# Performance work log

Measured on AMD Instinct MI355X. Metric: run time of the kernel, lower is better.

Reference implementation:

```python
import jax, jax.numpy as jnp
import numpy as np

B = 64
H_FS = W_FS = 56
IN_DIM, OUT_DIM, NUM_HEADS = 96, 192, 2
HEAD_DIM = OUT_DIM // NUM_HEADS  # 96
STRIDE_Q, STRIDE_KV = (2, 2), (4, 4)
REL_RANGE = 2 * (H_FS // STRIDE_Q[0]) - 1  # 55
LN_EPS = 1e-5


def setup_inputs() -> dict:
    key = jax.random.key(0)
    ks = jax.random.split(key, 12)
    N = H_FS * W_FS + 1  # +1 cls token
    s = 0.02
    d = {
        "hidden_states": jax.random.normal(ks[0], (B, N, IN_DIM), jnp.float32),
        "Wq": jax.random.normal(ks[1], (IN_DIM, OUT_DIM), jnp.float32) * s,
        "bq": jnp.zeros((OUT_DIM,), jnp.float32),
        "Wk": jax.random.normal(ks[2], (IN_DIM, OUT_DIM), jnp.float32) * s,
        "bk": jnp.zeros((OUT_DIM,), jnp.float32),
        "Wv": jax.random.normal(ks[3], (IN_DIM, OUT_DIM), jnp.float32) * s,
        "bv": jnp.zeros((OUT_DIM,), jnp.float32),
        # depthwise pool convs: (C_out=C, C_in/groups=1, kh, kw)
        "pool_q_w": jax.random.normal(ks[4], (IN_DIM, 1, 3, 3), jnp.float32) * 0.1,
        "pool_k_w": jax.random.normal(ks[5], (IN_DIM, 1, 3, 3), jnp.float32) * 0.1,
        "pool_v_w": jax.random.normal(ks[6], (IN_DIM, 1, 3, 3), jnp.float32) * 0.1,
        "gq": jnp.ones((IN_DIM,), jnp.float32), "betaq": jnp.zeros((IN_DIM,), jnp.float32),
        "gk": jnp.ones((IN_DIM,), jnp.float32), "betak": jnp.zeros((IN_DIM,), jnp.float32),
        "gv": jnp.ones((IN_DIM,), jnp.float32), "betav": jnp.zeros((IN_DIM,), jnp.float32),
        "rel_h": jax.random.normal(ks[7], (REL_RANGE, HEAD_DIM), jnp.float32) * s,
        "rel_w": jax.random.normal(ks[8], (REL_RANGE, HEAD_DIM), jnp.float32) * s,
        "height": H_FS,
        "width": W_FS,
    }
    return d


def _layernorm(x, g, b):
    m = x.mean(-1, keepdims=True)
    v = ((x - m) ** 2).mean(-1, keepdims=True)
    return (x - m) * jax.lax.rsqrt(v + LN_EPS) * g + b


def _pool(x, w, stride, g, b, height, width):
    # x: (B, folds=1, N, C) with cls token first
    bsz, _, _, C = x.shape
    cls_tok, rest = x[:, :, :1], x[:, :, 1:]
    sp = rest.reshape(bsz, height, width, C).transpose(0, 3, 1, 2)  # (B, C, H, W)
    y = jax.lax.conv_general_dilated(
        sp, w, stride, [(1, 1), (1, 1)], feature_group_count=C,
        dimension_numbers=("NCHW", "OIHW", "NCHW"))
    hp, wp = y.shape[2], y.shape[3]
    y = y.reshape(bsz, 1, C, hp * wp).transpose(0, 1, 3, 2)  # (B, 1, N', C)
    y = jnp.concatenate([cls_tok, y], axis=2)
    return _layernorm(y, g, b), (hp, wp)


def _rel_idx(qn, kn):
    q_ratio = max(kn / qn, 1.0)
    k_ratio = max(qn / kn, 1.0)
    dist = (np.arange(qn)[:, None] * q_ratio - np.arange(kn)[None, :] * k_ratio
            + (kn - 1) * k_ratio)
    return dist.astype(np.int64)


def reference(hidden_states, Wq, bq, Wk, bk, Wv, bv, pool_q_w, pool_k_w, pool_v_w,
              gq, betaq, gk, betak, gv, betav, rel_h, rel_w, height, width):
    bsz, N, C = hidden_states.shape
    h = hidden_states.reshape(bsz, N, 1, C).transpose(0, 2, 1, 3)  # (B, folds=1, N, C)

    q, (qh, qw) = _pool(h, pool_q_w, STRIDE_Q, gq, betaq, height, width)
    k, (kh, kw) = _pool(h, pool_k_w, STRIDE_KV, gk, betak, height, width)
    v, _ = _pool(h, pool_v_w, STRIDE_KV, gv, betav, height, width)

    def proj(x, W, bias, n):
        x = x.transpose(0, 2, 1, 3).reshape(bsz, n, -1)
        x = x @ W + bias
        return x.reshape(bsz, n, NUM_HEADS, HEAD_DIM).transpose(0, 2, 1, 3)

    nq, nk = qh * qw + 1, kh * kw + 1
    q = proj(q, Wq, bq, nq)  # (B, H, nq, d)
    k = proj(k, Wk, bk, nk)
    v = proj(v, Wv, bv, nk)

    scale = HEAD_DIM ** -0.5
    attn = jnp.einsum("bhqd,bhkd->bhqk", q * scale, k)

    # decomposed spatial relative positional bias (cls offset = 1)
    Rh = rel_h[_rel_idx(qh, kh)]  # (qh, kh, d)
    Rw = rel_w[_rel_idx(qw, kw)]  # (qw, kw, d)
    rq = q[:, :, 1:].reshape(bsz, NUM_HEADS, qh, qw, HEAD_DIM)
    eh = jnp.einsum("byhwc,hkc->byhwk", rq, Rh)
    ew = jnp.einsum("byhwc,wkc->byhwk", rq, Rw)
    blk = (attn[:, :, 1:, 1:].reshape(bsz, NUM_HEADS, qh, qw, kh, kw)
           + eh[..., :, None] + ew[..., None, :])
    attn = attn.at[:, :, 1:, 1:].set(blk.reshape(bsz, NUM_HEADS, qh * qw, kh * kw))

    attn = jax.nn.softmax(attn, axis=-1)
    out = jnp.einsum("bhqk,bhkd->bhqd", attn, v)
    out = out.at[:, :, 1:].add(q[:, :, 1:])  # residual pooling (skip cls)
    return out.transpose(0, 2, 1, 3).reshape(bsz, nq, OUT_DIM)
```

## Files before the change

### kernel.cpp

```cpp
#include <hip/hip_runtime.h>
#include <hip/hip_bf16.h>
#include <hip/hip_fp16.h>

#define B_    64
#define HFS   56
#define CIN   96
#define NQ    785
#define NK    197
#define QW    28
#define KW    14
#define NTOT  3137
#define NQP   800
#define NKP   208
#define NKPV  224
#define VROWS 112
#define KSCL  0.10206207261596575f
#define LOG2E 1.4426950408889634f
#define KSCL2 (KSCL*LOG2E)

typedef __attribute__((ext_vector_type(8))) short short8;
typedef __attribute__((ext_vector_type(4))) short shortx4;
typedef __attribute__((ext_vector_type(4))) float floatx4;

__device__ __forceinline__ short f2s(float x) {
    __hip_bfloat16 h = __float2bfloat16(x);
    return *reinterpret_cast<short*>(&h);
}
__device__ __forceinline__ float s2f(short s) {
    __hip_bfloat16 h; *reinterpret_cast<short*>(&h) = s;
    return __bfloat162float(h);
}
__device__ __forceinline__ short8 ld8(const short* p) {
    return *reinterpret_cast<const short8*>(p);
}
__device__ __forceinline__ unsigned pkbf(float a, float b) {
    return (unsigned)(unsigned short)f2s(a) | ((unsigned)(unsigned short)f2s(b) << 16);
}
__device__ __forceinline__ unsigned pkhf(float a, float b) {
    __half2 h = __floats2half2_rn(a, b);
    return *reinterpret_cast<unsigned*>(&h);
}
__device__ __forceinline__ float hflo(unsigned w) {
    __half2 h = *reinterpret_cast<__half2*>(&w);
    return __half2float(__low2half(h));
}
__device__ __forceinline__ float hfhi(unsigned w) {
    __half2 h = *reinterpret_cast<__half2*>(&w);
    return __half2float(__high2half(h));
}

#define MFMA16(a,b,c) __builtin_amdgcn_mfma_f32_16x16x32_bf16((a),(b),(c),0,0,0)

__global__ void prep_kernel(const float* __restrict__ Wq, const float* __restrict__ Wk,
                            const float* __restrict__ Wv, const float* __restrict__ relh,
                            const float* __restrict__ relw,
                            const float* __restrict__ pqw, const float* __restrict__ pkw,
                            const float* __restrict__ pvw,
                            short* __restrict__ WTq, short* __restrict__ WTk,
                            short* __restrict__ WTv, short* __restrict__ relc,
                            short* __restrict__ vt,
                            float* __restrict__ cwqT, float* __restrict__ cwkT,
                            float* __restrict__ cwvT)
{
    int i = blockIdx.x * 256 + threadIdx.x;
    if (i < 18432)      { int o = i/96, c = i%96;              WTq[o*96+c] = f2s(Wq[c*192+o]); }
    else if (i < 36864) { int j = i-18432; int o=j/96,c=j%96;  WTk[o*96+c] = f2s(Wk[c*192+o]*KSCL2); }
    else if (i < 55296) { int j = i-36864; int o=j/96,c=j%96;  WTv[o*96+c] = f2s(Wv[c*192+o]); }
    else if (i < 66048) {
        int j = i - 55296;  int r = j/96, c = j%96;
        float v = (r < 54) ? relh[r*96+c] : ((r < 108) ? relw[(r-54)*96+c] : 0.f);
        relc[r*96+c] = f2s(v*LOG2E);
    } else if (i < 721408) {
        int j2 = i - 66048;
        int bh = j2 / 5120, r = j2 % 5120;
        int row, tok; short val;
        if (r < 3584) { row = 96 + r/224; tok = r%224;
                        val = (row == 96 && tok < NK) ? (short)0x3F80 : (short)0; }
        else          { int rr = r-3584; row = rr/16; tok = 208 + (rr%16); val = 0; }
        vt[((long)bh*VROWS + row)*NKPV + tok] = val;
    } else if (i < 724000) {
        int j = i - 721408;
        int w = j / 864, r = j % 864;
        int c = r / 9, off = r % 9;
        const float* src = (w == 0) ? pqw : (w == 1) ? pkw : pvw;
        float*       dst = (w == 0) ? cwqT : (w == 1) ? cwkT : cwvT;
        dst[off*96 + c] = src[c*9 + off];
    }
}

__device__ __forceinline__ void red16_2(float& s, float& ss) {
    #pragma unroll
    for (int off = 8; off >= 1; off >>= 1) {
        s  += __shfl_xor(s,  off, 16);
        ss += __shfl_xor(ss, off, 16);
    }
}

__device__ __forceinline__ void ln6_store(const float* x, float m, float r,
    const float* __restrict__ g, const float* __restrict__ beta,
    int c0, short* __restrict__ outp)
{
    float2 g0 = *reinterpret_cast<const float2*>(g + c0);
    float2 g1 = *reinterpret_cast<const float2*>(g + c0 + 2);
    float2 g2 = *reinterpret_cast<const float2*>(g + c0 + 4);
    float2 b0 = *reinterpret_cast<const float2*>(beta + c0);
    float2 b1 = *reinterpret_cast<const float2*>(beta + c0 + 2);
    float2 b2 = *reinterpret_cast<const float2*>(beta + c0 + 4);
    unsigned o0 = pkbf((x[0]-m)*r*g0.x + b0.x, (x[1]-m)*r*g0.y + b0.y);
    unsigned o1 = pkbf((x[2]-m)*r*g1.x + b1.x, (x[3]-m)*r*g1.y + b1.y);
    unsigned o2 = pkbf((x[4]-m)*r*g2.x + b2.x, (x[5]-m)*r*g2.y + b2.y);
    *reinterpret_cast<unsigned*>(outp)     = o0;
    *reinterpret_cast<unsigned*>(outp + 2) = o1;
    *reinterpret_cast<unsigned*>(outp + 4) = o2;
}

__device__ __forceinline__ void zero6(short* __restrict__ outp) {
    *reinterpret_cast<unsigned*>(outp)     = 0u;
    *reinterpret_cast<unsigned*>(outp + 2) = 0u;
    *reinterpret_cast<unsigned*>(outp + 4) = 0u;
}

__global__ __launch_bounds__(256) void pool_ln_kernel(
    const float* __restrict__ hs,
    const float* __restrict__ cwqT, const float* __restrict__ cwkT, const float* __restrict__ cwvT,
    const float* __restrict__ gq, const float* __restrict__ betaq,
    const float* __restrict__ gk, const float* __restrict__ betak,
    const float* __restrict__ gv, const float* __restrict__ betav,
    short* __restrict__ pq, short* __restrict__ pk, short* __restrict__ pv)
{
    const int wid  = threadIdx.x >> 6;
    const int lane = threadIdx.x & 63;
    const int sub  = lane >> 4;
    const int li   = lane & 15;
    const int c0   = li * 6;
    const int gid  = blockIdx.x * 4 + wid;
    const int b    = gid / 252;
    const int slot = gid % 252;
    const long hb  = (long)b * NTOT * CIN;

    if (slot < 200) {
        int t = slot*4 + sub;
        short* outp = pq + ((long)b*NQP + t)*CIN + c0;
        if (t >= NQ) { zero6(outp); return; }
        float x[6];
        #pragma unroll
        for (int i = 0; i < 6; ++i) x[i] = 0.f;
        if (t == 0) {
            const float* hp = hs + hb + c0;
            float2 a0 = *reinterpret_cast<const float2*>(hp);
            float2 a1 = *reinterpret_cast<const float2*>(hp + 2);
            float2 a2 = *reinterpret_cast<const float2*>(hp + 4);
            x[0]=a0.x; x[1]=a0.y; x[2]=a1.x; x[3]=a1.y; x[4]=a2.x; x[5]=a2.y;
        } else {
            int j = t - 1, oy = j / QW, ox = j % QW;
            #pragma unroll
            for (int dy = 0; dy < 3; ++dy) {
                int iy = oy*2 - 1 + dy;
                #pragma unroll
                for (int dx = 0; dx < 3; ++dx) {
                    int ix = ox*2 - 1 + dx;
                    if (iy >= 0 && iy < HFS && ix >= 0 && ix < HFS) {
                        const float* hp = hs + hb + (long)(1 + iy*HFS + ix)*CIN + c0;
                        const float* wp = cwqT + (dy*3+dx)*96 + c0;
                        float2 h0 = *reinterpret_cast<const float2*>(hp);
                        float2 h1 = *reinterpret_cast<const float2*>(hp + 2);
                        float2 h2 = *reinterpret_cast<const float2*>(hp + 4);
                        float2 w0 = *reinterpret_cast<const float2*>(wp);
                        float2 w1 = *reinterpret_cast<const float2*>(wp + 2);
                        float2 w2 = *reinterpret_cast<const float2*>(wp + 4);
                        x[0] = fmaf(h0.x, w0.x, x[0]); x[1] = fmaf(h0.y, w0.y, x[1]);
                        x[2] = fmaf(h1.x, w1.x, x[2]); x[3] = fmaf(h1.y, w1.y, x[3]);
                        x[4] = fmaf(h2.x, w2.x, x[4]); x[5] = fmaf(h2.y, w2.y, x[5]);
                    }
                }
            }
        }
        float s  = (x[0]+x[1]) + (x[2]+x[3]) + (x[4]+x[5]);
        float ss = fmaf(x[0],x[0], fmaf(x[1],x[1], fmaf(x[2],x[2],
                   fmaf(x[3],x[3], fmaf(x[4],x[4], x[5]*x[5])))));
        red16_2(s, ss);
        float m   = s * (1.f/96.f);
        float var = ss * (1.f/96.f) - m*m;
        float r   = rsqrtf(var + 1e-5f);
        ln6_store(x, m, r, gq, betaq, c0, outp);
    } else {
        int tok = (slot - 200)*4 + sub;
        short* ok_ = pk + ((long)b*NKP + tok)*CIN + c0;
        short* ov_ = pv + ((long)b*NKP + tok)*CIN + c0;
        if (tok >= NK) { zero6(ok_); zero6(ov_); return; }
        float xk[6], xv[6];
        #pragma unroll
        for (int i = 0; i < 6; ++i) { xk[i] = 0.f; xv[i] = 0.f; }
        if (tok == 0) {
            const float* hp = hs + hb + c0;
            float2 a0 = *reinterpret_cast<const float2*>(hp);
            float2 a1 = *reinterpret_cast<const float2*>(hp + 2);
            float2 a2 = *reinterpret_cast<const float2*>(hp + 4);
            xk[0]=xv[0]=a0.x; xk[1]=xv[1]=a0.y; xk[2]=xv[2]=a1.x;
            xk[3]=xv[3]=a1.y; xk[4]=xv[4]=a2.x; xk[5]=xv[5]=a2.y;
        } else {
            int j = tok - 1, oy = j / KW, ox = j % KW;
            #pragma unroll
            for (int dy = 0; dy < 3; ++dy) {
                int iy = oy*4 - 1 + dy;
                #pragma unroll
                for (int dx = 0; dx < 3; ++dx) {
                    int ix = ox*4 - 1 + dx;
                    if (iy >= 0 && iy < HFS && ix >= 0 && ix < HFS) {
                        const float* hp = hs + hb + (long)(1 + iy*HFS + ix)*CIN + c0;
                        int wo = (dy*3+dx)*96 + c0;
                        float2 h0 = *reinterpret_cast<const float2*>(hp);
                        float2 h1 = *reinterpret_cast<const float2*>(hp + 2);
                        float2 h2 = *reinterpret_cast<const float2*>(hp + 4);
                        float2 k0 = *reinterpret_cast<const float2*>(cwkT + wo);
                        float2 k1 = *reinterpret_cast<const float2*>(cwkT + wo + 2);
                        float2 k2 = *reinterpret_cast<const float2*>(cwkT + wo + 4);
                        float2 v0 = *reinterpret_cast<const float2*>(cwvT + wo);
                        float2 v1 = *reinterpret_cast<const float2*>(cwvT + wo + 2);
                        float2 v2 = *reinterpret_cast<const float2*>(cwvT + wo + 4);
                        xk[0] = fmaf(h0.x, k0.x, xk[0]); xk[1] = fmaf(h0.y, k0.y, xk[1]);
                        xk[2] = fmaf(h1.x, k1.x, xk[2]); xk[3] = fmaf(h1.y, k1.y, xk[3]);
                        xk[4] = fmaf(h2.x, k2.x, xk[4]); xk[5] = fmaf(h2.y, k2.y, xk[5]);
                        xv[0] = fmaf(h0.x, v0.x, xv[0]); xv[1] = fmaf(h0.y, v0.y, xv[1]);
                        xv[2] = fmaf(h1.x, v1.x, xv[2]); xv[3] = fmaf(h1.y, v1.y, xv[3]);
                        xv[4] = fmaf(h2.x, v2.x, xv[4]); xv[5] = fmaf(h2.y, v2.y, xv[5]);
                    }
                }
            }
        }
        float sk  = (xk[0]+xk[1]) + (xk[2]+xk[3]) + (xk[4]+xk[5]);
        float ssk = fmaf(xk[0],xk[0], fmaf(xk[1],xk[1], fmaf(xk[2],xk[2],
                    fmaf(xk[3],xk[3], fmaf(xk[4],xk[4], xk[5]*xk[5])))));
        float sv  = (xv[0]+xv[1]) + (xv[2]+xv[3]) + (xv[4]+xv[5]);
        float ssv = fmaf(xv[0],xv[0], fmaf(xv[1],xv[1], fmaf(xv[2],xv[2],
                    fmaf(xv[3],xv[3], fmaf(xv[4],xv[4], xv[5]*xv[5])))));
        red16_2(sk, ssk);
        red16_2(sv, ssv);
        float mk = sk * (1.f/96.f), vark = ssk * (1.f/96.f) - mk*mk;
        float mv = sv * (1.f/96.f), varv = ssv * (1.f/96.f) - mv*mv;
        float rk = rsqrtf(vark + 1e-5f);
        float rv = rsqrtf(varv + 1e-5f);
        ln6_store(xk, mk, rk, gk, betak, c0, ok_);
        ln6_store(xv, mv, rv, gv, betav, c0, ov_);
    }
}

__global__ __launch_bounds__(256) void proj_mfma_kernel(
    const short* __restrict__ pq, const short* __restrict__ pk, const short* __restrict__ pv,
    const short* __restrict__ WTq, const short* __restrict__ WTk, const short* __restrict__ WTv,
    const float* __restrict__ bq, const float* __restrict__ bk, const float* __restrict__ bv,
    short* __restrict__ qb, short* __restrict__ kb, short* __restrict__ vt)
{
    int wid  = threadIdx.x >> 6;
    int lane = threadIdx.x & 63;
    int quad = lane >> 4, col = lane & 15;
    int wt = blockIdx.x * 4 + wid;

    if (wt < 2016) {
        const short *A, *WT; const float* bias; short* outp;
        int ntokp, row0; float bsc;
        if (wt < 1600) { A = pq; WT = WTq; bias = bq; outp = qb; ntokp = NQP; row0 = wt*32; bsc = 1.f; }
        else           { A = pk; WT = WTk; bias = bk; outp = kb; ntokp = NKP; row0 = (wt-1600)*32; bsc = KSCL2; }

        short8 bt[2][3];
        #pragma unroll
        for (int ti = 0; ti < 2; ++ti)
            #pragma unroll
            for (int cc = 0; cc < 3; ++cc)
                bt[ti][cc] = ld8(A + (long)(row0 + ti*16 + col)*96 + cc*32 + quad*8);

        int bT[2], tokT[2];
        #pragma unroll
        for (int ti = 0; ti < 2; ++ti) {
            int r = row0 + ti*16;
            bT[ti] = r / ntokp;
            tokT[ti] = (r % ntokp) + col;
        }

        short8 af[2][3];
        #pragma unroll
        for (int cc = 0; cc < 3; ++cc)
            af[0][cc] = ld8(WT + col*96 + cc*32 + quad*8);

        #pragma unroll
        for (int nt = 0; nt < 12; ++nt) {
            if (nt < 11) {
                #pragma unroll
                for (int cc = 0; cc < 3; ++cc)
                    af[(nt+1)&1][cc] = ld8(WT + ((nt+1)*16 + col)*96 + cc*32 + quad*8);
            }
            int o0 = nt*16 + quad*4;
            float4 bo = *reinterpret_cast<const float4*>(bias + o0);
            int h  = (o0 >= 96) ? 1 : 0;
            int d0 = o0 - h*96;
            #pragma unroll
            for (int ti = 0; ti < 2; ++ti) {
                floatx4 acc = {0.f, 0.f, 0.f, 0.f};
                #pragma unroll
                for (int cc = 0; cc < 3; ++cc)
                    acc = MFMA16(af[nt&1][cc], bt[ti][cc], acc);
                shortx4 val;
                val.x = f2s(acc[0] + bo.x*bsc);
                val.y = f2s(acc[1] + bo.y*bsc);
                val.z = f2s(acc[2] + bo.z*bsc);
                val.w = f2s(acc[3] + bo.w*bsc);
                *reinterpret_cast<shortx4*>(outp + ((long)(bT[ti]*2 + h)*ntokp + tokT[ti])*96 + d0) = val;
            }
        }
    } else {
        int row0 = (wt - 2016) * 32;
        short8 at[2][3];
        #pragma unroll
        for (int ti = 0; ti < 2; ++ti)
            #pragma unroll
            for (int cc = 0; cc < 3; ++cc)
                at[ti][cc] = ld8(pv + (long)(row0 + ti*16 + col)*96 + cc*32 + quad*8);

        int bT[2], t0T[2];
        #pragma unroll
        for (int ti = 0; ti < 2; ++ti) {
            int r = row0 + ti*16;
            bT[ti] = r / NKP;
            t0T[ti] = (r % NKP) + quad*4;
        }

        short8 bf[2][3];
        #pragma unroll
        for (int cc = 0; cc < 3; ++cc)
            bf[0][cc] = ld8(WTv + col*96 + cc*32 + quad*8);

        #pragma unroll
        for (int nt = 0; nt < 12; ++nt) {
            if (nt < 11) {
                #pragma unroll
                for (int cc = 0; cc < 3; ++cc)
                    bf[(nt+1)&1][cc] = ld8(WTv + ((nt+1)*16 + col)*96 + cc*32 + quad*8);
            }
            int o = nt*16 + col;
            int h = (o >= 96) ? 1 : 0;
            int d = o - h*96;
            float bo = bv[o];
            #pragma unroll
            for (int ti = 0; ti < 2; ++ti) {
                floatx4 acc = {0.f, 0.f, 0.f, 0.f};
                #pragma unroll
                for (int cc = 0; cc < 3; ++cc)
                    acc = MFMA16(at[ti][cc], bf[nt&1][cc], acc);
                shortx4 val;
                val.x = (t0T[ti]+0 < NK) ? f2s(acc[0] + bo) : (short)0;
                val.y = (t0T[ti]+1 < NK) ? f2s(acc[1] + bo) : (short)0;
                val.z = (t0T[ti]+2 < NK) ? f2s(acc[2] + bo) : (short)0;
                val.w = (t0T[ti]+3 < NK) ? f2s(acc[3] + bo) : (short)0;
                *reinterpret_cast<shortx4*>(vt + ((long)(bT[ti]*2 + h)*VROWS + d)*NKPV + t0T[ti]) = val;
            }
        }
    }
}

__global__ __launch_bounds__(64, 2) void attn_kernel(
    const short* __restrict__ qb, const short* __restrict__ kb,
    const short* __restrict__ vt, const short* __restrict__ relc,
    float* __restrict__ out)
{
    __shared__ __align__(16) short smem[2][16][232];

    int lane = threadIdx.x & 63;
    int quad = lane >> 4, col = lane & 15;

    int bid = blockIdx.x;
    int wt  = (bid & 7) * 400 + (bid >> 3);
    int bh  = wt / 25;
    int tp  = wt % 25;
    int q0  = tp * 32;

    const short* qrow = qb + ((long)bh*NQP + q0)*96;
    short8 aq[2][3];
    #pragma unroll
    for (int ti = 0; ti < 2; ++ti)
        #pragma unroll
        for (int c = 0; c < 3; ++c)
            aq[ti][c] = ld8(qrow + (ti*16 + col)*96 + c*32 + quad*8);

    short8 rf[2][3];
    #pragma unroll
    for (int c = 0; c < 3; ++c)
        rf[0][c] = ld8(relc + col*96 + c*32 + quad*8);
    #pragma unroll
    for (int rt = 0; rt < 7; ++rt) {
        if (rt < 6) {
            #pragma unroll
            for (int c = 0; c < 3; ++c)
                rf[(rt+1)&1][c] = ld8(relc + ((rt+1)*16 + col)*96 + c*32 + quad*8);
        }
        #pragma unroll
        for (int ti = 0; ti < 2; ++ti) {
            floatx4 acc = {0.f, 0.f, 0.f, 0.f};
            #pragma unroll
            for (int c = 0; c < 3; ++c)
                acc = MFMA16(aq[ti][c], rf[rt&1][c], acc);
            #pragma unroll
            for (int reg = 0; reg < 4; ++reg)
                smem[ti][quad*4 + reg][rt*16 + col] = f2s(acc[reg]);
        }
    }

    const short* kbase = kb + (long)bh*NKP*96;
    short8 kf[2][3];
    #pragma unroll
    for (int c = 0; c < 3; ++c)
        kf[0][c] = ld8(kbase + col*96 + c*32 + quad*8);

    int qyo[2][4], qxo[2][4];
    #pragma unroll
    for (int ti = 0; ti < 2; ++ti)
        #pragma unroll
        for (int reg = 0; reg < 4; ++reg) {
            int qq = q0 + ti*16 + quad*4 + reg;
            int jj = (qq > 0) ? (qq - 1) : 0;
            qyo[ti][reg] = jj / QW;
            qxo[ti][reg] = jj % QW;
        }

    unsigned bpk[2][13][2];
    #pragma unroll
    for (int kt = 0; kt < 13; ++kt) {
        int k  = kt*16 + col;
        int kk = (k > 0) ? (k - 1) : 0;
        int ky = kk / 14;  ky = (ky < 13) ? ky : 13;
        int kx = kk - 14*ky;
        int oh  = 26 - 2*ky;
        int ow2 = 26 - 2*kx;
        #pragma unroll
        for (int ti = 0; ti < 2; ++ti) {
            float bs[4];
            #pragma unroll
            for (int reg = 0; reg < 4; ++reg) {
                const short* er = &smem[ti][quad*4 + reg][0];
                float bias = s2f(er[qyo[ti][reg] + oh]) + s2f(er[54 + qxo[ti][reg] + ow2]);
                if (kt == 0) bias = (col == 0) ? 0.f : bias;
                if (q0 == 0 && ti == 0 && reg == 0) bias = (quad == 0) ? 0.f : bias;
                bs[reg] = bias;
            }
            bpk[ti][kt][0] = pkhf(bs[0], bs[1]);
            bpk[ti][kt][1] = pkhf(bs[2], bs[3]);
        }
    }

    const short* vbase = vt + (long)bh*VROWS*NKPV;
    short8 vf[2][7];
    #pragma unroll
    for (int kt = 0; kt < 13; ++kt) {
        if (kt < 12) {
            #pragma unroll
            for (int c = 0; c < 3; ++c)
                kf[(kt+1)&1][c] = ld8(kbase + ((kt+1)*16 + col)*96 + c*32 + quad*8);
        } else {
            #pragma unroll
            for (int nt = 0; nt < 7; ++nt)
                vf[0][nt] = ld8(vbase + (nt*16 + col)*NKPV + quad*8);
        }
        int k = kt*16 + col;
        __builtin_amdgcn_s_setprio(1);
        floatx4 accA = {0.f, 0.f, 0.f, 0.f};
        floatx4 accB = {0.f, 0.f, 0.f, 0.f};
        #pragma unroll
        for (int c = 0; c < 3; ++c) {
            accA = MFMA16(aq[0][c], kf[kt&1][c], accA);
            accB = MFMA16(aq[1][c], kf[kt&1][c], accB);
        }
        __builtin_amdgcn_s_setprio(0);
        unsigned a0 = bpk[0][kt][0], a1 = bpk[0][kt][1];
        unsigned b0 = bpk[1][kt][0], b1 = bpk[1][kt][1];
        smem[0][quad*4 + 0][k] = f2s(__builtin_amdgcn_exp2f(accA[0] + hflo(a0)));
        smem[0][quad*4 + 1][k] = f2s(__builtin_amdgcn_exp2f(accA[1] + hfhi(a0)));
        smem[0][quad*4 + 2][k] = f2s(__builtin_amdgcn_exp2f(accA[2] + hflo(a1)));
        smem[0][quad*4 + 3][k] = f2s(__builtin_amdgcn_exp2f(accA[3] + hfhi(a1)));
        smem[1][quad*4 + 0][k] = f2s(__builtin_amdgcn_exp2f(accB[0] + hflo(b0)));
        smem[1][quad*4 + 1][k] = f2s(__builtin_amdgcn_exp2f(accB[1] + hfhi(b0)));
        smem[1][quad*4 + 2][k] = f2s(__builtin_amdgcn_exp2f(accB[2] + hflo(b1)));
        smem[1][quad*4 + 3][k] = f2s(__builtin_amdgcn_exp2f(accB[3] + hfhi(b1)));
    }
    #pragma unroll
    for (int ti = 0; ti < 2; ++ti)
        #pragma unroll
        for (int reg = 0; reg < 4; ++reg)
            smem[ti][quad*4 + reg][208 + col] = 0;

    floatx4 o[2][7];
    #pragma unroll
    for (int ti = 0; ti < 2; ++ti)
        #pragma unroll
        for (int nt = 0; nt < 7; ++nt) o[ti][nt] = floatx4{0.f, 0.f, 0.f, 0.f};
    #pragma unroll
    for (int c = 0; c < 7; ++c) {
        if (c < 6) {
            #pragma unroll
            for (int nt = 0; nt < 7; ++nt)
                vf[(c+1)&1][nt] = ld8(vbase + (nt*16 + col)*NKPV + (c+1)*32 + quad*8);
        }
        short8 apA = ld8(&smem[0][col][c*32 + quad*8]);
        short8 apB = ld8(&smem[1][col][c*32 + quad*8]);
        __builtin_amdgcn_s_setprio(1);
        #pragma unroll
        for (int nt = 0; nt < 7; ++nt) {
            o[0][nt] = MFMA16(apA, vf[c&1][nt], o[0][nt]);
            o[1][nt] = MFMA16(apB, vf[c&1][nt], o[1][nt]);
        }
        __builtin_amdgcn_s_setprio(0);
    }

    float inv[2][4];
    #pragma unroll
    for (int ti = 0; ti < 2; ++ti)
        #pragma unroll
        for (int reg = 0; reg < 4; ++reg) {
            float srow = __shfl(o[ti][6][reg], lane & 48, 64);
            inv[ti][reg] = 1.0f / srow;
        }
    int b = bh >> 1, h = bh & 1;
    #pragma unroll
    for (int ti = 0; ti < 2; ++ti)
        #pragma unroll
        for (int nt = 0; nt < 6; ++nt) {
            int ch = nt*16 + col;
            #pragma unroll
            for (int reg = 0; reg < 4; ++reg) {
                int q = q0 + ti*16 + quad*4 + reg;
                if (q < NQ) {
                    float val = o[ti][nt][reg] * inv[ti][reg];
                    if (q > 0) val += s2f(qb[((long)bh*NQP + q)*96 + ch]);
                    out[((long)b*NQ + q)*192 + h*96 + ch] = val;
                }
            }
        }
}

extern "C" void kernel_launch(void* const* d_in, const int* in_sizes, int n_in,
                              void* d_out, int out_size, void* d_ws, size_t ws_size,
                              hipStream_t stream)
{
    const float* hs    = (const float*)d_in[0];
    const float* Wq    = (const float*)d_in[1];
    const float* bq    = (const float*)d_in[2];
    const float* Wk    = (const float*)d_in[3];
    const float* bk    = (const float*)d_in[4];
    const float* Wv    = (const float*)d_in[5];
    const float* bv    = (const float*)d_in[6];
    const float* pqw   = (const float*)d_in[7];
    const float* pkw   = (const float*)d_in[8];
    const float* pvw   = (const float*)d_in[9];
    const float* gq    = (const float*)d_in[10];
    const float* betaq = (const float*)d_in[11];
    const float* gk    = (const float*)d_in[12];
    const float* betak = (const float*)d_in[13];
    const float* gv    = (const float*)d_in[14];
    const float* betav = (const float*)d_in[15];
    const float* relh  = (const float*)d_in[16];
    const float* relw  = (const float*)d_in[17];
    float* out = (float*)d_out;

    short* pq   = (short*)d_ws;
    short* pk   = pq  + (long)B_*NQP*CIN;
    short* pv   = pk  + (long)B_*NKP*CIN;
    short* qb   = pv  + (long)B_*NKP*CIN;
    short* kb   = qb  + (long)128*NQP*96;
    short* vt   = kb  + (long)128*NKP*96;
    short* WTq  = vt  + (long)128*VROWS*NKPV;
    short* WTk  = WTq + 192*96;
    short* WTv  = WTk + 192*96;
    short* relc = WTv + 192*96;
    float* cwqT = (float*)(relc + 112*96);
    float* cwkT = cwqT + 9*96;
    float* cwvT = cwkT + 9*96;

    prep_kernel<<<2829, 256, 0, stream>>>(Wq, Wk, Wv, relh, relw,
                                          pqw, pkw, pvw,
                                          WTq, WTk, WTv, relc, vt,
                                          cwqT, cwkT, cwvT);

    pool_ln_kernel<<<(B_*1008)/16, 256, 0, stream>>>(
        hs, cwqT, cwkT, cwvT, gq, betaq, gk, betak, gv, betav, pq, pk, pv);

    proj_mfma_kernel<<<2432/4, 256, 0, stream>>>(
        pq, pk, pv, WTq, WTk, WTv, bq, bk, bv, qb, kb, vt);

    attn_kernel<<<3200, 64, 0, stream>>>(qb, kb, vt, relc, out);
}
```

Before: 241.4 us.

## Stage V tile in LDS shared by four waves and compute row sums in registers

```diff
diff --git a/kernel.cpp b/kernel.cpp
--- a/kernel.cpp
+++ b/kernel.cpp
@@ -12,8 +12,8 @@
 #define NTOT  3137
 #define NQP   800
 #define NKP   208
-#define NKPV  224
-#define VROWS 112
+#define VSTR  232
+#define VR    96
 #define KSCL  0.10206207261596575f
 #define LOG2E 1.4426950408889634f
 #define KSCL2 (KSCL*LOG2E)
@@ -70,16 +70,13 @@
         int j = i - 55296;  int r = j/96, c = j%96;
         float v = (r < 54) ? relh[r*96+c] : ((r < 108) ? relw[(r-54)*96+c] : 0.f);
         relc[r*96+c] = f2s(v*LOG2E);
-    } else if (i < 721408) {
+    } else if (i < 360960) {
         int j2 = i - 66048;
-        int bh = j2 / 5120, r = j2 % 5120;
-        int row, tok; short val;
-        if (r < 3584) { row = 96 + r/224; tok = r%224;
-                        val = (row == 96 && tok < NK) ? (short)0x3F80 : (short)0; }
-        else          { int rr = r-3584; row = rr/16; tok = 208 + (rr%16); val = 0; }
-        vt[((long)bh*VROWS + row)*NKPV + tok] = val;
-    } else if (i < 724000) {
-        int j = i - 721408;
+        int bh = j2 / 2304, r = j2 % 2304;
+        int row = r / 24, tok = 208 + (r % 24);
+        vt[(long)bh*(VR*VSTR) + row*VSTR + tok] = 0;
+    } else if (i < 363552) {
+        int j = i - 360960;
         int w = j / 864, r = j % 864;
         int c = r / 9, off = r % 9;
         const float* src = (w == 0) ? pqw : (w == 1) ? pkw : pvw;
@@ -351,188 +348,187 @@
                 val.y = (t0T[ti]+1 < NK) ? f2s(acc[1] + bo) : (short)0;
                 val.z = (t0T[ti]+2 < NK) ? f2s(acc[2] + bo) : (short)0;
                 val.w = (t0T[ti]+3 < NK) ? f2s(acc[3] + bo) : (short)0;
-                *reinterpret_cast<shortx4*>(vt + ((long)(bT[ti]*2 + h)*VROWS + d)*NKPV + t0T[ti]) = val;
+                *reinterpret_cast<shortx4*>(vt + ((long)(bT[ti]*2 + h)*VR + d)*VSTR + t0T[ti]) = val;
             }
         }
     }
 }
 
-__global__ __launch_bounds__(64, 2) void attn_kernel(
+__global__ __launch_bounds__(256, 2) void attn_kernel(
     const short* __restrict__ qb, const short* __restrict__ kb,
     const short* __restrict__ vt, const short* __restrict__ relc,
     float* __restrict__ out)
 {
-    __shared__ __align__(16) short smem[2][16][232];
-
-    int lane = threadIdx.x & 63;
+    __shared__ __align__(16) short Vlds[22528];
+    __shared__ __align__(16) short Plds[4][16][232];
+
+    int tid  = threadIdx.x;
+    int wid  = tid >> 6;
+    int lane = tid & 63;
     int quad = lane >> 4, col = lane & 15;
 
     int bid = blockIdx.x;
-    int wt  = (bid & 7) * 400 + (bid >> 3);
-    int bh  = wt / 25;
-    int tp  = wt % 25;
-    int q0  = tp * 32;
-
-    const short* qrow = qb + ((long)bh*NQP + q0)*96;
-    short8 aq[2][3];
+    int xcd = bid & 7, idx = bid >> 3;
+    int bh  = xcd*16 + idx/7;
+    int j   = idx % 7;
+    int unit = j*4 + wid;
+    bool active = (unit < 25);
+    int u  = active ? unit : 24;
+    int q0 = u * 32;
+
+    const short* vtg = vt + (long)bh * (VR*VSTR);
+    {
+        short8 tmp[11];
+        #pragma unroll
+        for (int t = 0; t < 11; ++t)
+            tmp[t] = ld8(vtg + (wid + t*4)*512 + lane*8);
+        #pragma unroll
+        for (int t = 0; t < 11; ++t)
+            *reinterpret_cast<short8*>(&Vlds[(wid + t*4)*512 + lane*8]) = tmp[t];
+    }
+
+    const short* kbase = kb + (long)bh*NKP*96;
+    int b = bh >> 1, h = bh & 1;
+
     #pragma unroll
-    for (int ti = 0; ti < 2; ++ti)
+    for (int ti = 0; ti < 2; ++ti) {
+        const short* qrow = qb + ((long)bh*NQP + q0 + ti*16)*96;
+        short8 aq[3];
         #pragma unroll
         for (int c = 0; c < 3; ++c)
-            aq[ti][c] = ld8(qrow + (ti*16 + col)*96 + c*32 + quad*8);
-
-    short8 rf[2][3];
-    #pragma unroll
-    for (int c = 0; c < 3; ++c)
-        rf[0][c] = ld8(relc + col*96 + c*32 + quad*8);
-    #pragma unroll
-    for (int rt = 0; rt < 7; ++rt) {
-        if (rt < 6) {
+            aq[c] = ld8(qrow + col*96 + c*32 + quad*8);
+
+        short8 rf[2][3];
+        #pragma unroll
+        for (int c = 0; c < 3; ++c)
+            rf[0][c] = ld8(relc + col*96 + c*32 + quad*8);
+        #pragma unroll
+        for (int rt = 0; rt < 7; ++rt) {
+            if (rt < 6) {
+                #pragma unroll
+                for (int c = 0; c < 3; ++c)
+                    rf[(rt+1)&1][c] = ld8(relc + ((rt+1)*16 + col)*96 + c*32 + quad*8);
+            }
+            floatx4 acc = {0.f, 0.f, 0.f, 0.f};
             #pragma unroll
             for (int c = 0; c < 3; ++c)
-                rf[(rt+1)&1][c] = ld8(relc + ((rt+1)*16 + col)*96 + c*32 + quad*8);
-        }
-        #pragma unroll
-        for (int ti = 0; ti < 2; ++ti) {
-            floatx4 acc = {0.f, 0.f, 0.f, 0.f};
-            #pragma unroll
-            for (int c = 0; c < 3; ++c)
-                acc = MFMA16(aq[ti][c], rf[rt&1][c], acc);
+                acc = MFMA16(aq[c], rf[rt&1][c], acc);
             #pragma unroll
             for (int reg = 0; reg < 4; ++reg)
-                smem[ti][quad*4 + reg][rt*16 + col] = f2s(acc[reg]);
-        }
-    }
-
-    const short* kbase = kb + (long)bh*NKP*96;
-    short8 kf[2][3];
-    #pragma unroll
-    for (int c = 0; c < 3; ++c)
-        kf[0][c] = ld8(kbase + col*96 + c*32 + quad*8);
-
-    int qyo[2][4], qxo[2][4];
-    #pragma unroll
-    for (int ti = 0; ti < 2; ++ti)
+                Plds[wid][quad*4 + reg][rt*16 + col] = f2s(acc[reg]);
+        }
+
+        int qyo[4], qxo[4];
         #pragma unroll
         for (int reg = 0; reg < 4; ++reg) {
             int qq = q0 + ti*16 + quad*4 + reg;
             int jj = (qq > 0) ? (qq - 1) : 0;
-            qyo[ti][reg] = jj / QW;
-            qxo[ti][reg] = jj % QW;
-        }
-
-    unsigned bpk[2][13][2];
-    #pragma unroll
-    for (int kt = 0; kt < 13; ++kt) {
-        int k  = kt*16 + col;
-        int kk = (k > 0) ? (k - 1) : 0;
-        int ky = kk / 14;  ky = (ky < 13) ? ky : 13;
-        int kx = kk - 14*ky;
-        int oh  = 26 - 2*ky;
-        int ow2 = 26 - 2*kx;
-        #pragma unroll
-        for (int ti = 0; ti < 2; ++ti) {
+            qyo[reg] = jj / QW;
+            qxo[reg] = jj % QW;
+        }
+
+        unsigned bpk[13][2];
+        #pragma unroll
+        for (int kt = 0; kt < 13; ++kt) {
+            int k  = kt*16 + col;
+            int kk = (k > 0) ? (k - 1) : 0;
+            int ky = kk / 14;  ky = (ky < 13) ? ky : 13;
+            int kx = kk - 14*ky;
+            int oh  = 26 - 2*ky;
+            int ow2 = 26 - 2*kx;
             float bs[4];
             #pragma unroll
             for (int reg = 0; reg < 4; ++reg) {
-                const short* er = &smem[ti][quad*4 + reg][0];
-                float bias = s2f(er[qyo[ti][reg] + oh]) + s2f(er[54 + qxo[ti][reg] + ow2]);
+                const short* er = &Plds[wid][quad*4 + reg][0];
+                float bias = s2f(er[qyo[reg] + oh]) + s2f(er[54 + qxo[reg] + ow2]);
                 if (kt == 0) bias = (col == 0) ? 0.f : bias;
                 if (q0 == 0 && ti == 0 && reg == 0) bias = (quad == 0) ? 0.f : bias;
                 bs[reg] = bias;
             }
-            bpk[ti][kt][0] = pkhf(bs[0], bs[1]);
-            bpk[ti][kt][1] = pkhf(bs[2], bs[3]);
-        }
-    }
-
-    const short* vbase = vt + (long)bh*VROWS*NKPV;
-    short8 vf[2][7];
-    #pragma unroll
-    for (int kt = 0; kt < 13; ++kt) {
-        if (kt < 12) {
+            bpk[kt][0] = pkhf(bs[0], bs[1]);
+            bpk[kt][1] = pkhf(bs[2], bs[3]);
+        }
+
+        float rsum[4] = {0.f, 0.f, 0.f, 0.f};
+        short8 kf[3][3];
+        #pragma unroll
+        for (int c = 0; c < 3; ++c)
+            kf[0][c] = ld8(kbase + col*96 + c*32 + quad*8);
+        #pragma unroll
+        for (int c = 0; c < 3; ++c)
+            kf[1][c] = ld8(kbase + (16 + col)*96 + c*32 + quad*8);
+        #pragma unroll
+        for (int kt = 0; kt < 13; ++kt) {
+            if (kt < 11) {
+                #pragma unroll
+                for (int c = 0; c < 3; ++c)
+                    kf[(kt+2)%3][c] = ld8(kbase + ((kt+2)*16 + col)*96 + c*32 + quad*8);
+            }
+            __builtin_amdgcn_s_setprio(1);
+            floatx4 acc = {0.f, 0.f, 0.f, 0.f};
             #pragma unroll
             for (int c = 0; c < 3; ++c)
-                kf[(kt+1)&1][c] = ld8(kbase + ((kt+1)*16 + col)*96 + c*32 + quad*8);
-        } else {
-            #pragma unroll
-            for (int nt = 0; nt < 7; ++nt)
-                vf[0][nt] = ld8(vbase + (nt*16 + col)*NKPV + quad*8);
-        }
-        int k = kt*16 + col;
-        __builtin_amdgcn_s_setprio(1);
-        floatx4 accA = {0.f, 0.f, 0.f, 0.f};
-        floatx4 accB = {0.f, 0.f, 0.f, 0.f};
-        #pragma unroll
-        for (int c = 0; c < 3; ++c) {
-            accA = MFMA16(aq[0][c], kf[kt&1][c], accA);
-            accB = MFMA16(aq[1][c], kf[kt&1][c], accB);
-        }
-        __builtin_amdgcn_s_setprio(0);
-        unsigned a0 = bpk[0][kt][0], a1 = bpk[0][kt][1];
-        unsigned b0 = bpk[1][kt][0], b1 = bpk[1][kt][1];
-        smem[0][quad*4 + 0][k] = f2s(__builtin_amdgcn_exp2f(accA[0] + hflo(a0)));
-        smem[0][quad*4 + 1][k] = f2s(__builtin_amdgcn_exp2f(accA[1] + hfhi(a0)));
-        smem[0][quad*4 + 2][k] = f2s(__builtin_amdgcn_exp2f(accA[2] + hflo(a1)));
-        smem[0][quad*4 + 3][k] = f2s(__builtin_amdgcn_exp2f(accA[3] + hfhi(a1)));
-        smem[1][quad*4 + 0][k] = f2s(__builtin_amdgcn_exp2f(accB[0] + hflo(b0)));
-        smem[1][quad*4 + 1][k] = f2s(__builtin_amdgcn_exp2f(accB[1] + hfhi(b0)));
-        smem[1][quad*4 + 2][k] = f2s(__builtin_amdgcn_exp2f(accB[2] + hflo(b1)));
-        smem[1][quad*4 + 3][k] = f2s(__builtin_amdgcn_exp2f(accB[3] + hfhi(b1)));
-    }
-    #pragma unroll
-    for (int ti = 0; ti < 2; ++ti)
+                acc = MFMA16(aq[c], kf[kt%3][c], acc);
+            __builtin_amdgcn_s_setprio(0);
+            int k = kt*16 + col;
+            unsigned w0 = bpk[kt][0], w1 = bpk[kt][1];
+            float e0 = __builtin_amdgcn_exp2f(acc[0] + hflo(w0));
+            float e1 = __builtin_amdgcn_exp2f(acc[1] + hfhi(w0));
+            float e2 = __builtin_amdgcn_exp2f(acc[2] + hflo(w1));
+            float e3 = __builtin_amdgcn_exp2f(acc[3] + hfhi(w1));
+            if (k >= NK) { e0 = 0.f; e1 = 0.f; e2 = 0.f; e3 = 0.f; }
+            Plds[wid][quad*4 + 0][k] = f2s(e0);
+            Plds[wid][quad*4 + 1][k] = f2s(e1);
+            Plds[wid][quad*4 + 2][k] = f2s(e2);
+            Plds[wid][quad*4 + 3][k] = f2s(e3);
+            rsum[0] += e0; rsum[1] += e1; rsum[2] += e2; rsum[3] += e3;
+        }
         #pragma unroll
         for (int reg = 0; reg < 4; ++reg)
-            smem[ti][quad*4 + reg][208 + col] = 0;
-
-    floatx4 o[2][7];
-    #pragma unroll
-    for (int ti = 0; ti < 2; ++ti)
-        #pragma unroll
-        for (int nt = 0; nt < 7; ++nt) o[ti][nt] = floatx4{0.f, 0.f, 0.f, 0.f};
-    #pragma unroll
-    for (int c = 0; c < 7; ++c) {
-        if (c < 6) {
-            #pragma unroll
-            for (int nt = 0; nt < 7; ++nt)
-                vf[(c+1)&1][nt] = ld8(vbase + (nt*16 + col)*NKPV + (c+1)*32 + quad*8);
-        }
-        short8 apA = ld8(&smem[0][col][c*32 + quad*8]);
-        short8 apB = ld8(&smem[1][col][c*32 + quad*8]);
-        __builtin_amdgcn_s_setprio(1);
-        #pragma unroll
-        for (int nt = 0; nt < 7; ++nt) {
-            o[0][nt] = MFMA16(apA, vf[c&1][nt], o[0][nt]);
-            o[1][nt] = MFMA16(apB, vf[c&1][nt], o[1][nt]);
-        }
-        __builtin_amdgcn_s_setprio(0);
-    }
-
-    float inv[2][4];
-    #pragma unroll
-    for (int ti = 0; ti < 2; ++ti)
+            Plds[wid][quad*4 + reg][208 + col] = 0;
+
+        float inv[4];
         #pragma unroll
         for (int reg = 0; reg < 4; ++reg) {
-            float srow = __shfl(o[ti][6][reg], lane & 48, 64);
-            inv[ti][reg] = 1.0f / srow;
-        }
-    int b = bh >> 1, h = bh & 1;
-    #pragma unroll
-    for (int ti = 0; ti < 2; ++ti)
+            float s = rsum[reg];
+            s += __shfl_xor(s, 1, 16);
+            s += __shfl_xor(s, 2, 16);
+            s += __shfl_xor(s, 4, 16);
+            s += __shfl_xor(s, 8, 16);
+            inv[reg] = 1.0f / s;
+        }
+
+        if (ti == 0) __syncthreads();
+
+        floatx4 o[6];
+        #pragma unroll
+        for (int nt = 0; nt < 6; ++nt) o[nt] = floatx4{0.f, 0.f, 0.f, 0.f};
+        #pragma unroll
+        for (int c = 0; c < 7; ++c) {
+            short8 pA = ld8(&Plds[wid][col][c*32 + quad*8]);
+            __builtin_amdgcn_s_setprio(1);
+            #pragma unroll
+            for (int nt = 0; nt < 6; ++nt) {
+                short8 vb = ld8(&Vlds[(nt*16 + col)*VSTR + c*32 + quad*8]);
+                o[nt] = MFMA16(pA, vb, o[nt]);
+            }
+            __builtin_amdgcn_s_setprio(0);
+        }
+
         #pragma unroll
         for (int nt = 0; nt < 6; ++nt) {
             int ch = nt*16 + col;
             #pragma unroll
             for (int reg = 0; reg < 4; ++reg) {
                 int q = q0 + ti*16 + quad*4 + reg;
-                if (q < NQ) {
-                    float val = o[ti][nt][reg] * inv[ti][reg];
+                if (active && q < NQ) {
+                    float val = o[nt][reg] * inv[reg];
                     if (q > 0) val += s2f(qb[((long)bh*NQP + q)*96 + ch]);
                     out[((long)b*NQ + q)*192 + h*96 + ch] = val;
                 }
             }
         }
+    }
 }
 
 extern "C" void kernel_launch(void* const* d_in, const int* in_sizes, int n_in,
@@ -565,7 +561,7 @@
     short* qb   = pv  + (long)B_*NKP*CIN;
     short* kb   = qb  + (long)128*NQP*96;
     short* vt   = kb  + (long)128*NKP*96;
-    short* WTq  = vt  + (long)128*VROWS*NKPV;
+    short* WTq  = vt  + (long)128*VR*VSTR;
     short* WTk  = WTq + 192*96;
     short* WTv  = WTk + 192*96;
     short* relc = WTv + 192*96;
@@ -573,7 +569,7 @@
     float* cwkT = cwqT + 9*96;
     float* cwvT = cwkT + 9*96;
 
-    prep_kernel<<<2829, 256, 0, stream>>>(Wq, Wk, Wv, relh, relw,
+    prep_kernel<<<1421, 256, 0, stream>>>(Wq, Wk, Wv, relh, relw,
                                           pqw, pkw, pvw,
                                           WTq, WTk, WTv, relc, vt,
                                           cwqT, cwkT, cwvT);
@@ -584,5 +580,5 @@
     proj_mfma_kernel<<<2432/4, 256, 0, stream>>>(
         pq, pk, pv, WTq, WTk, WTv, bq, bk, bv, qb, kb, vt);
 
-    attn_kernel<<<3200, 64, 0, stream>>>(qb, kb, vt, relc, out);
-}
+    attn_kernel<<<896, 256, 0, stream>>>(qb, kb, vt, relc, out);
+}
```

Measured after the change: 249.3 us. 1.03x slower.
